# Kernel tuning notes

Measured on AMD Instinct MI355X. Metric: run time of the kernel, lower is better.

Reference implementation:

```python
import jax, jax.numpy as jnp
import numpy as np

B, C, H, W = 16, 64, 64, 64  # z_e shape; C == embedding_dim
K = 1024                     # num_embeddings
COMMITMENT_COST = 0.25
EPS = 1e-5


def setup_inputs() -> dict:
    key = jax.random.key(0)
    k1, k2 = jax.random.split(key)
    z_e = jax.random.normal(k1, (B, C, H, W), dtype=jnp.float32)
    # codebook init ~ U(-1/D, 1/D) as in the torch module
    emb_w = jax.random.uniform(k2, (K, C), dtype=jnp.float32, minval=-1.0 / C, maxval=1.0 / C)
    return {"z_e": z_e, "emb_w": emb_w}


def reference(z_e, emb_w):
    orig_dtype = z_e.dtype
    b, c, h, w = z_e.shape
    z = z_e.astype(jnp.float32)
    # per-channel std over (batch, h, w); computed under no_grad in torch -> stop_gradient
    std = jax.lax.stop_gradient(
        jnp.clip(jnp.std(z, axis=(0, 2, 3), keepdims=True, ddof=1), EPS, None)
    )
    z = z / std                                        # [b,c,h,w]
    zf = z.transpose(0, 2, 3, 1).reshape(-1, c)        # [N, c]
    ew = emb_w.astype(jnp.float32)                     # [K, c]
    # squared euclidean distances: ||z||^2 - 2 z.e + ||e||^2  -> [N, K]
    d = (
        jnp.sum(zf * zf, axis=1, keepdims=True)
        - 2.0 * (zf @ ew.T)
        + jnp.sum(ew * ew, axis=1)
    )
    idx = jnp.argmin(d, axis=1)                        # [N]
    z_q = ew[idx].reshape(b, h, w, c).transpose(0, 3, 1, 2)  # [b,c,h,w]
    z_sg = jax.lax.stop_gradient(z)
    commitment = COMMITMENT_COST * jnp.mean((z_sg - z_q) ** 2)
    codebook = jnp.mean((z_sg - z_q) ** 2)             # eval-mode codebook loss
    vq_loss = commitment + codebook
    z_q_st = (z + jax.lax.stop_gradient(z_q - z)).astype(orig_dtype)
    n_tokens = idx.shape[0]
    counts = jnp.zeros((K,), dtype=jnp.float32).at[idx].add(1.0)
    avg_probs = counts / n_tokens
    perplexity = jnp.exp(-jnp.sum(avg_probs * jnp.log(jnp.clip(avg_probs, 1e-10, None))))
    indices = idx.reshape(b, h, w)
    return z_q_st, vq_loss, perplexity, indices
```

## Files before the change

kernel.cpp:

```cpp
#include <hip/hip_runtime.h>
#include <math.h>
#include <float.h>

#define HW 4096
#define CHW 262144
#define NTOK 65536
#define NELEM 4194304

#define WS_LOSS 0
#define WS_PART 1024
#define WS_EE   2048
#define WS_E2   3072
#define WS_HIST 68608
#define WS_DONE 69632

#define EPSM 1.0e-4f

typedef __attribute__((ext_vector_type(8))) short bf16x8;
typedef __attribute__((ext_vector_type(4))) float f32x4;

__device__ __forceinline__ unsigned short f2bf(float x) {
  unsigned u = __float_as_uint(x);
  u += 0x7FFFu + ((u >> 16) & 1u);
  return (unsigned short)(u >> 16);
}
__device__ __forceinline__ float bf2f(unsigned short h) {
  return __uint_as_float(((unsigned)h) << 16);
}
__device__ __forceinline__ void gload_lds16(const unsigned short* g, unsigned short* l) {
  __builtin_amdgcn_global_load_lds(
      (const __attribute__((address_space(1))) unsigned int*)g,
      (__attribute__((address_space(3))) unsigned int*)l, 16, 0, 0);
}

__global__ __launch_bounds__(1024) void k_pre(const float* __restrict__ z,
                                              const float* __restrict__ emb,
                                              double* __restrict__ part,
                                              unsigned short* __restrict__ e2g,
                                              float* __restrict__ eeg,
                                              int* __restrict__ hist,
                                              int* __restrict__ done) {
  __shared__ double rs[16], rs2[16];
  int tid = threadIdx.x;
  int blk = blockIdx.x;
  if (blk == 0 && tid == 0) *done = 0;
  if (blk < 256) {
    int c = blk & 63, q = blk >> 6;
    double s = 0.0, s2 = 0.0;
    const float* base = z + (size_t)c * HW;
    #pragma unroll
    for (int jj = 0; jj < 4; ++jj) {
      int bb = (q << 2) + jj;
      float4 v = *(const float4*)(base + (size_t)bb * CHW + (tid << 2));
      s  += (double)v.x + (double)v.y + (double)v.z + (double)v.w;
      s2 += (double)v.x * v.x + (double)v.y * v.y + (double)v.z * v.z + (double)v.w * v.w;
    }
    for (int o = 32; o > 0; o >>= 1) {
      s += __shfl_down(s, o, 64);
      s2 += __shfl_down(s2, o, 64);
    }
    int wv = tid >> 6, ln = tid & 63;
    if (ln == 0) { rs[wv] = s; rs2[wv] = s2; }
    __syncthreads();
    if (tid == 0) {
      double S = 0.0, S2 = 0.0;
      #pragma unroll
      for (int w = 0; w < 16; ++w) { S += rs[w]; S2 += rs2[w]; }
      part[(c << 2) + q] = S;
      part[256 + (c << 2) + q] = S2;
    }
  } else {
    int ct = blk - 256;
    if (ct == 0) hist[tid] = 0;
    int k0 = ct << 6;
    int code = tid >> 4, c4 = tid & 15;
    float4 v = *(const float4*)(emb + (size_t)((k0 + code) << 6) + (c4 << 2));
    unsigned short h0 = f2bf(v.x), h1 = f2bf(v.y), h2 = f2bf(v.z), h3 = f2bf(v.w);
    unsigned short l0 = f2bf(v.x - bf2f(h0)), l1 = f2bf(v.y - bf2f(h1));
    unsigned short l2 = f2bf(v.z - bf2f(h2)), l3 = f2bf(v.w - bf2f(h3));
    int jL = (c4 >> 1) & 3;
    int e = (c4 & 1) << 2;
    int cH = code >> 4, cL = code & 15;
    size_t base = (size_t)ct * 8192 + cH * 512 + jL * 128 + cL * 8 + e;
    int jHh = c4 >> 3;
    *(uint2*)(e2g + base + (size_t)jHh * 2048) =
        make_uint2((unsigned)h0 | ((unsigned)h1 << 16), (unsigned)h2 | ((unsigned)h3 << 16));
    *(uint2*)(e2g + base + (size_t)(2 + jHh) * 2048) =
        make_uint2((unsigned)l0 | ((unsigned)l1 << 16), (unsigned)l2 | ((unsigned)l3 << 16));
    if (tid < 64) {
      const float* er = emb + (size_t)((k0 + tid) << 6);
      float s = 0.f;
      #pragma unroll
      for (int c = 0; c < 64; ++c) s = fmaf(er[c], er[c], s);
      eeg[k0 + tid] = s;
    }
  }
}

__global__ __launch_bounds__(256, 2) void k_vq(
    const float* __restrict__ z_e, const float* __restrict__ emb,
    const double* __restrict__ part, const float* __restrict__ eeg,
    const unsigned short* __restrict__ e2g,
    float* __restrict__ out_zq, float* __restrict__ out_idx,
    float* __restrict__ loss_part, int* __restrict__ done,
    float* __restrict__ out_scalars, int* __restrict__ hist) {
  __shared__ unsigned short A2[8192];
  __shared__ unsigned short B2[8192];
  __shared__ float sRstd[64];
  __shared__ double rl[4], rh[4];
  __shared__ int lastFlag;
  float* hs1 = (float*)A2;
  float* hs2 = (float*)A2 + 256;
  float* hs3 = (float*)A2 + 512;
  int*   hk1 = (int*)A2 + 768;
  int*   hk2 = (int*)A2 + 1024;
  int*   skf = (int*)A2 + 1280;
  int*   mk2f = (int*)A2 + 1344;
  int*   pairL = (int*)A2 + 1408;
  int*   fullL = (int*)A2 + 1472;
  int*   cntB = (int*)A2 + 1536;
  int*   cntC = (int*)A2 + 1537;
  float* sred = (float*)A2 + 1540;
  float* zf   = (float*)A2 + 1544;
  float* fbd4 = (float*)A2 + 1608;
  int*   fbk4 = (int*)A2 + 1612;

  int tid = threadIdx.x;
  int lane = tid & 63;
  int wv = tid >> 6;
  int blk = blockIdx.x;
  int b = blk >> 6;
  int s0 = (blk & 63) << 6;

  if (tid < 64) {
    double S = 0.0, S2 = 0.0;
    #pragma unroll
    for (int q = 0; q < 4; ++q) {
      S += part[(tid << 2) + q];
      S2 += part[256 + (tid << 2) + q];
    }
    const double N = (double)NTOK;
    double var = (S2 - S * S / N) / (N - 1.0);
    float sd = fmaxf((float)sqrt(var), 1e-5f);
    sRstd[tid] = 1.0f / sd;
  }
  __syncthreads();

  {
    int t = tid & 63, q = tid >> 6;
    int half = q >> 1, jl0 = (q & 1) << 1;
    const float* zsrc = z_e + (size_t)b * CHW + (size_t)(q << 4) * HW + s0 + t;
    unsigned hw_[8], lw_[8];
    #pragma unroll
    for (int cc = 0; cc < 16; ++cc) {
      float v = zsrc[(size_t)cc * HW] * sRstd[(q << 4) + cc];
      unsigned short h = f2bf(v);
      unsigned short l = f2bf(v - bf2f(h));
      if (cc & 1) { hw_[cc >> 1] |= ((unsigned)h) << 16; lw_[cc >> 1] |= ((unsigned)l) << 16; }
      else        { hw_[cc >> 1] = h;                    lw_[cc >> 1] = l; }
    }
    int base = (t >> 4) * 512 + (t & 15) * 8;
    #pragma unroll
    for (int u = 0; u < 2; ++u) {
      *(uint4*)(A2 + half * 2048 + base + (jl0 + u) * 128) =
          make_uint4(hw_[4 * u], hw_[4 * u + 1], hw_[4 * u + 2], hw_[4 * u + 3]);
      *(uint4*)(A2 + (2 + half) * 2048 + base + (jl0 + u) * 128) =
          make_uint4(lw_[4 * u], lw_[4 * u + 1], lw_[4 * u + 2], lw_[4 * u + 3]);
    }
  }

  int quad = lane >> 4, l15 = lane & 15;

  {
    const unsigned short* gsrc = e2g + wv * 512 + (lane << 3);
    unsigned short* ldst = B2 + wv * 512;
    #pragma unroll
    for (int rr = 0; rr < 4; ++rr)
      gload_lds16(gsrc + rr * 2048, ldst + rr * 2048);
  }
  __syncthreads();

  bf16x8 afc[4][4];
  #pragma unroll
  for (int j = 0; j < 4; ++j)
    #pragma unroll
    for (int mt = 0; mt < 4; ++mt)
      afc[j][mt] = *(const bf16x8*)(A2 + j * 2048 + mt * 512 + quad * 128 + l15 * 8);
  __syncthreads();

  float ts1[16], ts2[16], ts3[16];
  int tk1[16], tk2[16];
  #pragma unroll
  for (int i = 0; i < 16; ++i) { ts1[i] = FLT_MAX; ts2[i] = FLT_MAX; ts3[i] = FLT_MAX; tk1[i] = 0; tk2[i] = 0; }

  const int aJH[8] = {0, 1, 2, 3, 0, 1, 2, 3};
  const int bJH[8] = {0, 1, 0, 1, 2, 3, 2, 3};

  #pragma unroll 1
  for (int ct = 0; ct < 16; ++ct) {
    const unsigned short* bb = (ct & 1) ? A2 : B2;
    if (ct < 15) {
      const unsigned short* gsrc = e2g + (size_t)(ct + 1) * 8192 + wv * 512 + (lane << 3);
      unsigned short* ldst = (((ct + 1) & 1) ? A2 : B2) + wv * 512;
      #pragma unroll
      for (int rr = 0; rr < 4; ++rr)
        gload_lds16(gsrc + rr * 2048, ldst + rr * 2048);
    }
    float ee0 = eeg[(ct << 6) + (wv << 4) + l15];

    f32x4 acc[4];
    #pragma unroll
    for (int mt = 0; mt < 4; ++mt) acc[mt] = (f32x4)(0.f);

    #pragma unroll
    for (int s = 0; s < 8; ++s) {
      bf16x8 bfr = *(const bf16x8*)(bb + bJH[s] * 2048 + wv * 512 + quad * 128 + l15 * 8);
      #pragma unroll
      for (int mt = 0; mt < 4; ++mt)
        acc[mt] = __builtin_amdgcn_mfma_f32_16x16x32_bf16(afc[aJH[s]][mt], bfr, acc[mt], 0, 0, 0);
    }

    int kc = (ct << 6) + (wv << 4) + l15;
    #pragma unroll
    for (int mt = 0; mt < 4; ++mt) {
      #pragma unroll
      for (int r = 0; r < 4; ++r) {
        float sv = fmaf(-2.0f, acc[mt][r], ee0);
        int sl = (mt << 2) + r;
        bool lt1 = sv < ts1[sl];
        bool lt2 = sv < ts2[sl];
        bool lt3 = sv < ts3[sl];
        ts3[sl] = lt2 ? ts2[sl] : (lt3 ? sv : ts3[sl]);
        tk2[sl] = lt1 ? tk1[sl] : (lt2 ? kc : tk2[sl]);
        ts2[sl] = lt1 ? ts1[sl] : (lt2 ? sv : ts2[sl]);
        tk1[sl] = lt1 ? kc : tk1[sl];
        ts1[sl] = lt1 ? sv : ts1[sl];
      }
    }
    if (ct < 15) __syncthreads();
  }
  __syncthreads();

  #pragma unroll
  for (int m = 1; m <= 8; m <<= 1) {
    #pragma unroll
    for (int sl = 0; sl < 16; ++sl) {
      float ob1 = __shfl_xor(ts1[sl], m, 64); int oq1 = __shfl_xor(tk1[sl], m, 64);
      float ob2 = __shfl_xor(ts2[sl], m, 64); int oq2 = __shfl_xor(tk2[sl], m, 64);
      float ob3 = __shfl_xor(ts3[sl], m, 64);
      bool t1 = (ts1[sl] < ob1) || (ts1[sl] == ob1 && tk1[sl] < oq1);
      float o1 = t1 ? ts1[sl] : ob1; int ok1 = t1 ? tk1[sl] : oq1;
      float aH = t1 ? ts2[sl] : ts1[sl]; int aHk = t1 ? tk2[sl] : tk1[sl]; float aH2 = t1 ? ts3[sl] : ts2[sl];
      float bH = t1 ? ob1 : ob2;         int bHk = t1 ? oq1 : oq2;         float bH2 = t1 ? ob2 : ob3;
      bool t2 = (aH < bH) || (aH == bH && aHk < bHk);
      float o2 = t2 ? aH : bH; int ok2 = t2 ? aHk : bHk;
      float aI = t2 ? aH2 : aH;
      float bI = t2 ? bH : bH2;
      ts1[sl] = o1; tk1[sl] = ok1; ts2[sl] = o2; tk2[sl] = ok2; ts3[sl] = fminf(aI, bI);
    }
  }
  if (tid == 0) { *cntB = 0; *cntC = 0; }
  if (l15 == 0) {
    #pragma unroll
    for (int mt = 0; mt < 4; ++mt)
      #pragma unroll
      for (int r = 0; r < 4; ++r) {
        int t = (mt << 4) + (quad << 2) + r;
        int sl = (mt << 2) + r;
        hs1[(wv << 6) + t] = ts1[sl]; hs2[(wv << 6) + t] = ts2[sl]; hs3[(wv << 6) + t] = ts3[sl];
        hk1[(wv << 6) + t] = tk1[sl]; hk2[(wv << 6) + t] = tk2[sl];
      }
  }
  __syncthreads();

  if (tid < 64) {
    float a1 = hs1[tid], a2 = hs2[tid], a3 = hs3[tid];
    int e1 = hk1[tid], e2v = hk2[tid];
    #pragma unroll
    for (int w = 1; w < 4; ++w) {
      float b1 = hs1[(w << 6) + tid], b2 = hs2[(w << 6) + tid], b3 = hs3[(w << 6) + tid];
      int f1 = hk1[(w << 6) + tid], f2 = hk2[(w << 6) + tid];
      bool t1 = (a1 < b1) || (a1 == b1 && e1 < f1);
      float o1 = t1 ? a1 : b1; int ok1 = t1 ? e1 : f1;
      float aH = t1 ? a2 : a1; int aHk = t1 ? e2v : e1; float aH2 = t1 ? a3 : a2;
      float bH = t1 ? b1 : b2; int bHk = t1 ? f1 : f2; float bH2 = t1 ? b2 : b3;
      bool t2 = (aH < bH) || (aH == bH && aHk < bHk);
      a1 = o1; e1 = ok1;
      a2 = t2 ? aH : bH; e2v = t2 ? aHk : bHk;
      a3 = fminf(t2 ? aH2 : aH, t2 ? bH : bH2);
    }
    skf[tid] = e1;
    mk2f[tid] = e2v;
    if (a2 - a1 <= EPSM) {
      if (a3 - a1 > EPSM) { int p = atomicAdd(cntB, 1); pairL[p] = tid; }
      else                { int p = atomicAdd(cntC, 1); fullL[p] = tid; }
    }
  }
  __syncthreads();

  int nB = *cntB, nC = *cntC;

  if (tid < nB) {
    int t = pairL[tid];
    int ka = skf[t], kb = mk2f[t];
    const float* za = z_e + (size_t)b * CHW + s0 + t;
    const float* ea = emb + ((size_t)ka << 6);
    const float* ebp = emb + ((size_t)kb << 6);
    float zz = 0.f, da = 0.f, db = 0.f;
    #pragma unroll
    for (int c = 0; c < 64; ++c) {
      float zv = za[(size_t)c * HW] * sRstd[c];
      zz = fmaf(zv, zv, zz);
      da = fmaf(ea[c], zv, da);
      db = fmaf(ebp[c], zv, db);
    }
    float d1 = (zz - 2.0f * da) + eeg[ka];
    float d2 = (zz - 2.0f * db) + eeg[kb];
    if (d2 < d1 || (d2 == d1 && kb < ka)) skf[t] = kb;
  }
  __syncthreads();

  for (int i = 0; i < nC; ++i) {
    int t = fullL[i];
    if (tid < 64) zf[tid] = z_e[(size_t)b * CHW + (size_t)tid * HW + s0 + t] * sRstd[tid];
    __syncthreads();
    const float4* zf4 = (const float4*)zf;
    const float* er0 = emb + ((size_t)(tid << 2) << 6);
    float zz = 0.f;
    float dot[4] = {0.f, 0.f, 0.f, 0.f};
    #pragma unroll
    for (int c4 = 0; c4 < 16; ++c4) {
      float4 zv = zf4[c4];
      zz = fmaf(zv.x, zv.x, zz); zz = fmaf(zv.y, zv.y, zz);
      zz = fmaf(zv.z, zv.z, zz); zz = fmaf(zv.w, zv.w, zz);
      #pragma unroll
      for (int j = 0; j < 4; ++j) {
        float4 ev = *(const float4*)(er0 + (j << 6) + (c4 << 2));
        dot[j] = fmaf(ev.x, zv.x, dot[j]);
        dot[j] = fmaf(ev.y, zv.y, dot[j]);
        dot[j] = fmaf(ev.z, zv.z, dot[j]);
        dot[j] = fmaf(ev.w, zv.w, dot[j]);
      }
    }
    float bdl = FLT_MAX; int bkl = 0;
    #pragma unroll
    for (int j = 0; j < 4; ++j) {
      float dd = (zz - 2.0f * dot[j]) + eeg[(tid << 2) + j];
      if (dd < bdl) { bdl = dd; bkl = (tid << 2) + j; }
    }
    #pragma unroll
    for (int m = 1; m <= 32; m <<= 1) {
      float od = __shfl_xor(bdl, m, 64);
      int   ok = __shfl_xor(bkl, m, 64);
      if (od < bdl || (od == bdl && ok < bkl)) { bdl = od; bkl = ok; }
    }
    if (lane == 0) { fbd4[wv] = bdl; fbk4[wv] = bkl; }
    __syncthreads();
    if (tid == 0) {
      float bb2 = fbd4[0]; int kk2 = fbk4[0];
      #pragma unroll
      for (int w = 1; w < 4; ++w)
        if (fbd4[w] < bb2 || (fbd4[w] == bb2 && fbk4[w] < kk2)) { bb2 = fbd4[w]; kk2 = fbk4[w]; }
      skf[t] = kk2;
    }
    __syncthreads();
  }
  __syncthreads();

  if (tid < 64) {
    int k = skf[tid];
    out_idx[(blk << 6) + tid] = (float)k;
    atomicAdd(&hist[k], 1);
  }

  {
    int t = tid & 63;
    int g = tid >> 6;
    int kq = skf[t];
    const float* eq = emb + ((size_t)kq << 6) + (g << 4);
    const float* zb2 = z_e + (size_t)b * CHW + (size_t)(g << 4) * HW + s0 + t;
    float* ob = out_zq + (size_t)b * CHW + (size_t)(g << 4) * HW + s0 + t;
    float lsum = 0.f;
    #pragma unroll
    for (int j4 = 0; j4 < 4; ++j4) {
      float4 ev = *(const float4*)(eq + (j4 << 2));
      #pragma unroll
      for (int u = 0; u < 4; ++u) {
        int jj = (j4 << 2) + u;
        float zv = zb2[(size_t)jj * HW] * sRstd[(g << 4) + jj];
        float e = (&ev.x)[u];
        float df = zv - e;
        lsum = fmaf(df, df, lsum);
        ob[(size_t)jj * HW] = zv + (e - zv);
      }
    }
    for (int o = 32; o > 0; o >>= 1) lsum += __shfl_down(lsum, o, 64);
    if (lane == 0) sred[wv] = lsum;
  }
  __syncthreads();

  if (tid == 0) {
    loss_part[blk] = sred[0] + sred[1] + sred[2] + sred[3];
    __threadfence();
    int prev = atomicAdd(done, 1);
    lastFlag = (prev == 1023);
  }
  __syncthreads();
  if (!lastFlag) return;

  double ls = (double)loss_part[tid] + (double)loss_part[tid + 256]
            + (double)loss_part[tid + 512] + (double)loss_part[tid + 768];
  double hsum = 0.0;
  #pragma unroll
  for (int jj = 0; jj < 4; ++jj) {
    float p = (float)hist[tid + (jj << 8)] * (1.0f / 65536.0f);
    float lg = logf(fmaxf(p, 1e-10f));
    hsum += (double)(p * lg);
  }
  for (int o = 32; o > 0; o >>= 1) {
    ls += __shfl_down(ls, o, 64);
    hsum += __shfl_down(hsum, o, 64);
  }
  if (lane == 0) { rl[wv] = ls; rh[wv] = hsum; }
  __syncthreads();
  if (tid == 0) {
    double L = rl[0] + rl[1] + rl[2] + rl[3];
    double Hn = rh[0] + rh[1] + rh[2] + rh[3];
    float m = (float)(L / (double)NELEM);
    out_scalars[0] = 0.25f * m + m;
    out_scalars[1] = expf((float)(-Hn));
  }
}

extern "C" void kernel_launch(void* const* d_in, const int* in_sizes, int n_in,
                              void* d_out, int out_size, void* d_ws, size_t ws_size,
                              hipStream_t stream) {
  const float* z_e = (const float*)d_in[0];
  const float* emb = (const float*)d_in[1];
  float* ws = (float*)d_ws;
  float* loss_part = ws + WS_LOSS;
  double* part = (double*)(ws + WS_PART);
  float* eeg = ws + WS_EE;
  unsigned short* e2g = (unsigned short*)(ws + WS_E2);
  int* hist = (int*)(ws + WS_HIST);
  int* done = (int*)(ws + WS_DONE);

  float* out = (float*)d_out;
  float* out_zq = out;
  float* out_scalars = out + NELEM;
  float* out_idx = out + NELEM + 2;

  k_pre<<<272, 1024, 0, stream>>>(z_e, emb, part, e2g, eeg, hist, done);
  k_vq<<<1024, 256, 0, stream>>>(z_e, emb, part, eeg, e2g, out_zq, out_idx,
                                 loss_part, done, out_scalars, hist);
}
```

Before: 194.1 us.

## Pack tile index into distance bits and truncate K-reduction MFMA steps

Encodes the codebook tile index in the low 4 mantissa bits of each biased distance, so the top-3 tracking becomes branchless fminf/fmaxf chains with no index registers. The ||e||^2 table is staged in LDS with a +8 offset to keep distances positive. The number of MFMA steps per tile drops from 8 to 6, which skips a quarter of the z·e products. The screening margin EPSM is widened to compensate. This cuts VALU work and MFMA count, but it computes an approximate dot product and risks wrong argmin choices unless a later exact rescoring catches every case.

```diff
diff --git a/kernel.cpp b/kernel.cpp
--- a/kernel.cpp
+++ b/kernel.cpp
@@ -14,7 +14,7 @@
 #define WS_HIST 68608
 #define WS_DONE 69632
 
-#define EPSM 1.0e-4f
+#define EPSM 2.0e-4f
 
 typedef __attribute__((ext_vector_type(8))) short bf16x8;
 typedef __attribute__((ext_vector_type(4))) float f32x4;
@@ -106,6 +106,7 @@
     float* __restrict__ out_scalars, int* __restrict__ hist) {
   __shared__ unsigned short A2[8192];
   __shared__ unsigned short B2[8192];
+  __shared__ float sEE[1024];
   __shared__ float sRstd[64];
   __shared__ double rl[4], rh[4];
   __shared__ int lastFlag;
@@ -132,6 +133,12 @@
   int b = blk >> 6;
   int s0 = (blk & 63) << 6;
 
+  {
+    float4 ev = ((const float4*)eeg)[tid];
+    ev.x += 8.0f; ev.y += 8.0f; ev.z += 8.0f; ev.w += 8.0f;
+    ((float4*)sEE)[tid] = ev;
+  }
+
   if (tid < 64) {
     double S = 0.0, S2 = 0.0;
     #pragma unroll
@@ -189,12 +196,11 @@
   __syncthreads();
 
   float ts1[16], ts2[16], ts3[16];
-  int tk1[16], tk2[16];
   #pragma unroll
-  for (int i = 0; i < 16; ++i) { ts1[i] = FLT_MAX; ts2[i] = FLT_MAX; ts3[i] = FLT_MAX; tk1[i] = 0; tk2[i] = 0; }
-
-  const int aJH[8] = {0, 1, 2, 3, 0, 1, 2, 3};
-  const int bJH[8] = {0, 1, 0, 1, 2, 3, 2, 3};
+  for (int i = 0; i < 16; ++i) { ts1[i] = FLT_MAX; ts2[i] = FLT_MAX; ts3[i] = FLT_MAX; }
+
+  const int aJH[6] = {0, 1, 2, 3, 0, 1};
+  const int bJH[6] = {0, 1, 0, 1, 2, 3};
 
   #pragma unroll 1
   for (int ct = 0; ct < 16; ++ct) {
@@ -206,40 +212,50 @@
       for (int rr = 0; rr < 4; ++rr)
         gload_lds16(gsrc + rr * 2048, ldst + rr * 2048);
     }
-    float ee0 = eeg[(ct << 6) + (wv << 4) + l15];
+    float ee0 = sEE[(ct << 6) + (wv << 4) + l15];
 
     f32x4 acc[4];
     #pragma unroll
     for (int mt = 0; mt < 4; ++mt) acc[mt] = (f32x4)(0.f);
 
     #pragma unroll
-    for (int s = 0; s < 8; ++s) {
+    for (int s = 0; s < 6; ++s) {
       bf16x8 bfr = *(const bf16x8*)(bb + bJH[s] * 2048 + wv * 512 + quad * 128 + l15 * 8);
       #pragma unroll
       for (int mt = 0; mt < 4; ++mt)
         acc[mt] = __builtin_amdgcn_mfma_f32_16x16x32_bf16(afc[aJH[s]][mt], bfr, acc[mt], 0, 0, 0);
     }
 
-    int kc = (ct << 6) + (wv << 4) + l15;
+    unsigned ctu = (unsigned)ct;
     #pragma unroll
     for (int mt = 0; mt < 4; ++mt) {
       #pragma unroll
       for (int r = 0; r < 4; ++r) {
         float sv = fmaf(-2.0f, acc[mt][r], ee0);
+        sv = fmaxf(sv, 0.25f);
+        float p = __uint_as_float((__float_as_uint(sv) & 0xFFFFFFF0u) | ctu);
         int sl = (mt << 2) + r;
-        bool lt1 = sv < ts1[sl];
-        bool lt2 = sv < ts2[sl];
-        bool lt3 = sv < ts3[sl];
-        ts3[sl] = lt2 ? ts2[sl] : (lt3 ? sv : ts3[sl]);
-        tk2[sl] = lt1 ? tk1[sl] : (lt2 ? kc : tk2[sl]);
-        ts2[sl] = lt1 ? ts1[sl] : (lt2 ? sv : ts2[sl]);
-        tk1[sl] = lt1 ? kc : tk1[sl];
-        ts1[sl] = lt1 ? sv : ts1[sl];
+        float t1o = ts1[sl], t2o = ts2[sl];
+        ts1[sl] = fminf(p, t1o);
+        ts2[sl] = fminf(fmaxf(p, t1o), t2o);
+        ts3[sl] = fminf(fmaxf(p, t2o), ts3[sl]);
       }
     }
     if (ct < 15) __syncthreads();
   }
   __syncthreads();
+
+  int tk1[16], tk2[16];
+  #pragma unroll
+  for (int sl = 0; sl < 16; ++sl) {
+    unsigned b1 = __float_as_uint(ts1[sl]);
+    unsigned b2 = __float_as_uint(ts2[sl]);
+    tk1[sl] = (int)(((b1 & 15u) << 6) | ((unsigned)wv << 4) | (unsigned)l15);
+    tk2[sl] = (int)(((b2 & 15u) << 6) | ((unsigned)wv << 4) | (unsigned)l15);
+    ts1[sl] = __uint_as_float(b1 & ~15u);
+    ts2[sl] = __uint_as_float(b2 & ~15u);
+    ts3[sl] = __uint_as_float(__float_as_uint(ts3[sl]) & ~15u);
+  }
 
   #pragma unroll
   for (int m = 1; m <= 8; m <<= 1) {
```

Result: no change. 193.0 us (-0.6%).
